# Kernel optimization log

Hardware: AMD Instinct MI355X
Metric: run time of the kernel (lower is better)

Reference implementation:

```python
import jax, jax.numpy as jnp
import numpy as np


def setup_inputs() -> dict:
    key = jax.random.key(0)
    k1, k2, k3, k4 = jax.random.split(key, 4)
    B, S, D = 2, 2048, 1024
    return {
        "X": jax.random.normal(k1, (B, S, D), dtype=jnp.float32),
        "W_q": jax.random.normal(k2, (D, D), dtype=jnp.float32),
        "W_k": jax.random.normal(k3, (D, D), dtype=jnp.float32),
        "W_v": jax.random.normal(k4, (D, D), dtype=jnp.float32),
        "n_heads": 16,
    }


def reference(X, W_q, W_k, W_v, n_heads):
    B, S, D = X.shape
    H = n_heads
    dh = D // H
    # QKV projections, split heads: [B,S,D] -> [H,B,S,dh]
    def split_heads(Y):
        return Y.reshape(B, S, H, dh).transpose(2, 0, 1, 3)
    Q = split_heads(X @ W_q)
    K = split_heads(X @ W_k)
    V = split_heads(X @ W_v)
    scale = 1.0 / jnp.sqrt(jnp.asarray(dh, dtype=X.dtype))
    # [H,B,S,S] attention scores (naive, matches the original)
    scores = jax.nn.softmax(jnp.einsum("hbqd,hbkd->hbqk", Q, K) * scale, axis=-1)
    out = jnp.einsum("hbqk,hbkd->hbqd", scores, V)  # [H,B,S,dh]
    # torch.concat(out, 0) over leading H dim -> [H*B, S, dh]
    return out.reshape(H * B, S, dh)
```

## Files before the change

### kernel.cpp

```cpp
#include <hip/hip_runtime.h>

typedef unsigned short u16;
typedef unsigned int u32;
typedef __bf16 bf16x8 __attribute__((ext_vector_type(8)));
typedef float f32x4 __attribute__((ext_vector_type(4)));
typedef float f32x16 __attribute__((ext_vector_type(16)));

extern "C" __device__ float __ocml_native_exp2_f32(float);

#define WT_HI_E  ((size_t)0)
#define WT_LO_E  ((size_t)3 << 20)
#define X_HI_E   ((size_t)6 << 20)
#define X_LO_E   ((size_t)10 << 20)
#define Q_HI_E   ((size_t)14 << 20)
#define Q_LO_E   ((size_t)18 << 20)
#define K_HI_E   ((size_t)22 << 20)
#define K_LO_E   ((size_t)26 << 20)
#define V_HI_E   ((size_t)30 << 20)

__device__ __forceinline__ u16 bf16_rne(float x) {
  u32 u = __float_as_uint(x);
  u32 r = (u + 0x7fffu + ((u >> 16) & 1u)) >> 16;
  return (u16)r;
}
__device__ __forceinline__ float bf16_f(u16 h) {
  return __uint_as_float(((u32)h) << 16);
}
__device__ __forceinline__ u16 f2bf(float x) {
  __bf16 b = (__bf16)x;
  return __builtin_bit_cast(u16, b);
}

__device__ __forceinline__ void gload16(const u16* g, u16* l) {
  __builtin_amdgcn_global_load_lds(
      (const __attribute__((address_space(1))) void*)g,
      (__attribute__((address_space(3))) void*)l, 16, 0, 0);
}

__global__ __launch_bounds__(256) void k_split(const float* __restrict__ X,
                                               const float* __restrict__ w0,
                                               const float* __restrict__ w1,
                                               const float* __restrict__ w2,
                                               u16* __restrict__ ws) {
  int bid = blockIdx.x;
  if (bid < 2048) {
    u16* xh = ws + X_HI_E;
    u16* xl = ws + X_LO_E;
    size_t i = ((size_t)bid * 256 + threadIdx.x) * 8;
    float4 a = *(const float4*)(X + i);
    float4 b = *(const float4*)(X + i + 4);
    float v[8] = {a.x, a.y, a.z, a.w, b.x, b.y, b.z, b.w};
    u32 Hh[4], Ll[4];
#pragma unroll
    for (int j = 0; j < 4; j++) {
      u16 h0 = f2bf(v[2 * j]);
      u16 h1 = f2bf(v[2 * j + 1]);
      u16 l0 = f2bf(v[2 * j] - bf16_f(h0));
      u16 l1 = f2bf(v[2 * j + 1] - bf16_f(h1));
      Hh[j] = (u32)h0 | ((u32)h1 << 16);
      Ll[j] = (u32)l0 | ((u32)l1 << 16);
    }
    *(uint4*)(xh + i) = make_uint4(Hh[0], Hh[1], Hh[2], Hh[3]);
    *(uint4*)(xl + i) = make_uint4(Ll[0], Ll[1], Ll[2], Ll[3]);
  } else {
    int wb = bid - 2048;
    int z = wb >> 8;
    int rem = wb & 255;
    int by = (rem >> 4) * 64, bx = (rem & 15) * 64;
    const float* W = (z == 0) ? w0 : ((z == 1) ? w1 : w2);
    u16* th = ws + WT_HI_E + (size_t)z * (1u << 20);
    u16* tl = ws + WT_LO_E + (size_t)z * (1u << 20);
    __shared__ float tile[64][65];
    int tx = threadIdx.x & 15, ty = threadIdx.x >> 4;
#pragma unroll
    for (int i = 0; i < 4; i++) {
      int r = ty + i * 16;
      float4 v = *(const float4*)(W + (size_t)(by + r) * 1024 + bx + tx * 4);
      tile[r][tx * 4 + 0] = v.x;
      tile[r][tx * 4 + 1] = v.y;
      tile[r][tx * 4 + 2] = v.z;
      tile[r][tx * 4 + 3] = v.w;
    }
    __syncthreads();
#pragma unroll
    for (int p = 0; p < 2; p++) {
      int t = threadIdx.x + 256 * p;
      int kc = t & 7, nl = t >> 3;
      u32 Hh[4], Ll[4];
#pragma unroll
      for (int u = 0; u < 4; u++) {
        float v0 = tile[kc * 8 + 2 * u][nl];
        float v1 = tile[kc * 8 + 2 * u + 1][nl];
        u16 h0 = f2bf(v0);
        u16 h1 = f2bf(v1);
        u16 l0 = f2bf(v0 - bf16_f(h0));
        u16 l1 = f2bf(v1 - bf16_f(h1));
        Hh[u] = (u32)h0 | ((u32)h1 << 16);
        Ll[u] = (u32)l0 | ((u32)l1 << 16);
      }
      size_t o = (size_t)(bx + nl) * 1024 + by + kc * 8;
      *(uint4*)(th + o) = make_uint4(Hh[0], Hh[1], Hh[2], Hh[3]);
      *(uint4*)(tl + o) = make_uint4(Ll[0], Ll[1], Ll[2], Ll[3]);
    }
  }
}

__global__ __launch_bounds__(256, 4) void k_proj(u16* __restrict__ ws) {
  int id = blockIdx.x;
  int xcd = id & 7;
  int loc = id >> 3;
  int m_loc = loc & 7;
  int rest = loc >> 3;
  int n_blk = rest & 7, z = rest >> 3;
  int M0 = (xcd * 8 + m_loc) * 64;
  int N0 = n_blk * 128;

  const u16* Xh = ws + X_HI_E;
  const u16* Xl = ws + X_LO_E;
  const u16* Wh = ws + WT_HI_E + (size_t)z * (1u << 20);
  const u16* Wl = ws + WT_LO_E + (size_t)z * (1u << 20);
  u16* dsth = ws + ((z == 0) ? Q_HI_E : ((z == 1) ? K_HI_E : V_HI_E));
  u16* dstl = (z == 0) ? (ws + Q_LO_E) : ((z == 1) ? (ws + K_LO_E) : (u16*)0);

  __shared__ u16 smem[12288];
  u16* sXh = smem;
  u16* sXl = smem + 2048;
  u16* sWh = smem + 4096;
  u16* sWl = smem + 8192;

  int tid = threadIdx.x, lane = tid & 63, w = tid >> 6;
  int quad = lane >> 4, l16 = lane & 15;
  int mb = (w & 1) * 32, nb = (w >> 1) * 64;

  const f32x4 z4 = {0.f, 0.f, 0.f, 0.f};
  f32x4 acc[4][2];
#pragma unroll
  for (int j = 0; j < 4; j++)
#pragma unroll
    for (int i = 0; i < 2; i++) acc[j][i] = z4;

  int xrow = tid >> 2, xq8 = tid & 3;

  for (int kk = 0; kk < 1024; kk += 32) {
    __syncthreads();
    {
      size_t gx = (size_t)(M0 + xrow) * 1024 + kk + xq8 * 8;
      gload16(Xh + gx, &sXh[(size_t)(w * 16) * 32]);
      if (z != 2) gload16(Xl + gx, &sXl[(size_t)(w * 16) * 32]);
#pragma unroll
      for (int j = 0; j < 2; j++) {
        int c = tid + 256 * j;
        int row = c >> 2, q8 = c & 3;
        size_t gw = (size_t)(N0 + row) * 1024 + kk + q8 * 8;
        gload16(Wh + gw, &sWh[(size_t)(j * 64 + w * 16) * 32]);
        if (z != 2) gload16(Wl + gw, &sWl[(size_t)(j * 64 + w * 16) * 32]);
      }
    }
    __syncthreads();
    bf16x8 ah[2], bh[4];
#pragma unroll
    for (int i = 0; i < 2; i++)
      ah[i] = *(const bf16x8*)&sXh[(mb + i * 16 + l16) * 32 + quad * 8];
#pragma unroll
    for (int j = 0; j < 4; j++)
      bh[j] = *(const bf16x8*)&sWh[(nb + j * 16 + l16) * 32 + quad * 8];
    if (z != 2) {
      bf16x8 al[2], bl[4];
#pragma unroll
      for (int i = 0; i < 2; i++)
        al[i] = *(const bf16x8*)&sXl[(mb + i * 16 + l16) * 32 + quad * 8];
#pragma unroll
      for (int j = 0; j < 4; j++)
        bl[j] = *(const bf16x8*)&sWl[(nb + j * 16 + l16) * 32 + quad * 8];
#pragma unroll
      for (int j = 0; j < 4; j++)
#pragma unroll
        for (int i = 0; i < 2; i++) {
          f32x4 c0 = acc[j][i];
          c0 = __builtin_amdgcn_mfma_f32_16x16x32_bf16(bh[j], ah[i], c0, 0, 0, 0);
          c0 = __builtin_amdgcn_mfma_f32_16x16x32_bf16(bh[j], al[i], c0, 0, 0, 0);
          c0 = __builtin_amdgcn_mfma_f32_16x16x32_bf16(bl[j], ah[i], c0, 0, 0, 0);
          acc[j][i] = c0;
        }
    } else {
#pragma unroll
      for (int j = 0; j < 4; j++)
#pragma unroll
        for (int i = 0; i < 2; i++)
          acc[j][i] = __builtin_amdgcn_mfma_f32_16x16x32_bf16(ah[i], bh[j], acc[j][i], 0, 0, 0);
    }
  }

  __syncthreads();
  int b = M0 >> 11, S0 = M0 & 2047;

  if (z != 2) {
    u16* my = smem + (size_t)w * 2048;
    int hh = (N0 + nb) >> 6;
    int sbase = S0 + mb;
    float qscale = (z == 0) ? (0.125f * 1.4426950408889634f) : 1.0f;
#pragma unroll
    for (int pass = 0; pass < 2; pass++) {
      u16* dst = pass ? dstl : dsth;
#pragma unroll
      for (int j = 0; j < 4; j++)
#pragma unroll
        for (int i = 0; i < 2; i++) {
          int dl = j * 16 + quad * 4;
          int sl = i * 16 + l16;
          u16 e[4];
#pragma unroll
          for (int r = 0; r < 4; r++) {
            float y = acc[j][i][r] * qscale;
            u16 hv = bf16_rne(y);
            e[r] = pass ? bf16_rne(y - bf16_f(hv)) : hv;
          }
          int elem = sl * 64 + (((dl >> 3) ^ (sl & 7)) << 3) + (dl & 7);
          *(uint2*)&my[elem] = make_uint2((u32)e[0] | ((u32)e[1] << 16),
                                          (u32)e[2] | ((u32)e[3] << 16));
        }
#pragma unroll
      for (int t = 0; t < 4; t++) {
        int sr = (lane >> 3) + t * 8;
        int p = lane & 7;
        int rc = (z == 1) ? p : (p ^ (sr & 7));
        uint4 v = *(const uint4*)&my[sr * 64 + rc * 8];
        size_t o = ((size_t)(hh * 2 + b) * 2048 + sbase + sr) * 64 + p * 8;
        *(uint4*)&dst[o] = v;
      }
    }
  } else {
#pragma unroll
    for (int j = 0; j < 4; j++)
#pragma unroll
      for (int i = 0; i < 2; i++) {
        int dl = j * 16 + l16;
        int s64 = mb + i * 16 + quad * 4;
        u16 e[4];
#pragma unroll
        for (int r = 0; r < 4; r++) e[r] = bf16_rne(acc[j][i][r]);
        int cp = ((s64 >> 3) & 7) ^ (dl & 7);
        int elem = (w >> 1) * 4096 + dl * 64 + (cp << 3) + (s64 & 7);
        *(uint2*)&smem[elem] = make_uint2((u32)e[0] | ((u32)e[1] << 16),
                                          (u32)e[2] | ((u32)e[3] << 16));
      }
    __syncthreads();
    int half = w >> 1;
    int hh = (N0 + half * 64) >> 6;
#pragma unroll
    for (int t = 0; t < 4; t++) {
      int dr = (w & 1) * 32 + (lane >> 3) + t * 8;
      int p = lane & 7;
      uint4 v = *(const uint4*)&smem[half * 4096 + dr * 64 + p * 8];
      size_t o = ((size_t)(hh * 2 + b) * 64 + dr) * 2048 + S0 + p * 8;
      *(uint4*)&dsth[o] = v;
    }
  }
}

__global__ __launch_bounds__(256, 2) void k_attn(u16* __restrict__ ws,
                                                 float* __restrict__ out) {
  const u16* Qh = ws + Q_HI_E;
  const u16* Ql = ws + Q_LO_E;
  const u16* Kh = ws + K_HI_E;
  const u16* Kl = ws + K_LO_E;
  const u16* Vt = ws + V_HI_E;

  __shared__ u16 sKh[2][64][64], sKl[2][64][64], sVt[2][64][64];

  int id = blockIdx.x;
  int hb = id & 31, qb = id >> 5;
  int tid = threadIdx.x, w = tid >> 6, lane = tid & 63;
  int l31 = lane & 31, h = lane >> 5;
  size_t base = (size_t)hb * (2048 * 64);
  int qw0 = qb * 128 + w * 32;

  int srow = lane >> 3, sch = lane & 7;

  auto stage = [&](int buf, int kt) {
#pragma unroll
    for (int b2 = 0; b2 < 2; b2++) {
      int rr = w * 16 + b2 * 8;
      size_t kg = base + (size_t)(kt + rr + srow) * 64 + sch * 8;
      gload16(Kh + kg, &sKh[buf][rr][0]);
      gload16(Kl + kg, &sKl[buf][rr][0]);
      size_t vg = base + (size_t)(rr + srow) * 2048 + kt + sch * 8;
      gload16(Vt + vg, &sVt[buf][rr][0]);
    }
  };

  stage(0, 0);

  bf16x8 qh[4], ql[4];
#pragma unroll
  for (int ks = 0; ks < 4; ks++) {
    size_t off = base + (size_t)(qw0 + l31) * 64 + ks * 16 + h * 8;
    qh[ks] = *(const bf16x8*)(Qh + off);
    ql[ks] = *(const bf16x8*)(Ql + off);
  }

  f32x16 o[2];
#pragma unroll
  for (int i = 0; i < 16; i++) { o[0][i] = 0.f; o[1][i] = 0.f; }
  float mr = -1e30f, lr = 0.f;

  auto rdA = [&](const u16 t[64][64], int mt, int ks) -> bf16x8 {
    int ch = ((ks * 2 + h) ^ (l31 & 7)) * 8;
    return *(const bf16x8*)&t[mt * 32 + l31][ch];
  };

  for (int it = 0; it < 32; it++) {
    __syncthreads();
    if (it + 1 < 32) stage((it + 1) & 1, (it + 1) * 64);
    int buf = it & 1;

    f32x16 sc[2];
#pragma unroll
    for (int i = 0; i < 16; i++) { sc[0][i] = 0.f; sc[1][i] = 0.f; }
#pragma unroll
    for (int ks = 0; ks < 4; ks++)
#pragma unroll
      for (int mt = 0; mt < 2; mt++) {
        bf16x8 kh = rdA(sKh[buf], mt, ks);
        bf16x8 kl = rdA(sKl[buf], mt, ks);
        sc[mt] = __builtin_amdgcn_mfma_f32_32x32x16_bf16(kh, qh[ks], sc[mt], 0, 0, 0);
        sc[mt] = __builtin_amdgcn_mfma_f32_32x32x16_bf16(kh, ql[ks], sc[mt], 0, 0, 0);
        sc[mt] = __builtin_amdgcn_mfma_f32_32x32x16_bf16(kl, qh[ks], sc[mt], 0, 0, 0);
      }

    float mx = sc[0][0];
#pragma unroll
    for (int i = 0; i < 16; i++) {
      mx = fmaxf(mx, sc[0][i]);
      mx = fmaxf(mx, sc[1][i]);
    }
    mx = fmaxf(mx, __shfl_xor(mx, 32));
    float mnew = fmaxf(mr, mx);
    float alpha = __ocml_native_exp2_f32(mr - mnew);
    mr = mnew;
    float rs = 0.f;
    u32 pk[2][8];
#pragma unroll
    for (int t = 0; t < 2; t++)
#pragma unroll
      for (int i = 0; i < 8; i++) {
        float p0 = __ocml_native_exp2_f32(sc[t][2 * i] - mnew);
        float p1 = __ocml_native_exp2_f32(sc[t][2 * i + 1] - mnew);
        rs += p0 + p1;
        u32 a = __float_as_uint(p0) + 0x8000u;
        u32 b = __float_as_uint(p1) + 0x8000u;
        pk[t][i] = __builtin_amdgcn_perm(b, a, 0x07060302u);
      }
    rs += __shfl_xor(rs, 32);
    lr = lr * alpha + rs;
#pragma unroll
    for (int i = 0; i < 16; i++) {
      o[0][i] *= alpha;
      o[1][i] *= alpha;
    }

#pragma unroll
    for (int ks = 0; ks < 4; ks++) {
      int t = ks >> 1, c = ks & 1;
      u32 b0 = pk[t][c * 4 + 0], b1 = pk[t][c * 4 + 1];
      u32 b2 = pk[t][c * 4 + 2], b3 = pk[t][c * 4 + 3];
      u32 rA = (u32)__shfl_xor((int)(h ? b0 : b2), 32);
      u32 rB = (u32)__shfl_xor((int)(h ? b1 : b3), 32);
      uint4 fb = h ? make_uint4(rA, rB, b2, b3) : make_uint4(b0, b1, rA, rB);
      bf16x8 pfrag = *(bf16x8*)&fb;
#pragma unroll
      for (int mt = 0; mt < 2; mt++) {
        bf16x8 vb = rdA(sVt[buf], mt, ks);
        o[mt] = __builtin_amdgcn_mfma_f32_32x32x16_bf16(vb, pfrag, o[mt], 0, 0, 0);
      }
    }
  }

  float inv = 1.f / lr;
  size_t grow = (size_t)hb * 2048 + qw0 + l31;
#pragma unroll
  for (int mt = 0; mt < 2; mt++)
#pragma unroll
    for (int g2 = 0; g2 < 4; g2++) {
      int d0 = mt * 32 + g2 * 8 + 4 * h;
      float4 v = make_float4(o[mt][g2 * 4 + 0] * inv, o[mt][g2 * 4 + 1] * inv,
                             o[mt][g2 * 4 + 2] * inv, o[mt][g2 * 4 + 3] * inv);
      *(float4*)(out + grow * 64 + d0) = v;
    }
}

extern "C" void kernel_launch(void* const* d_in, const int* in_sizes, int n_in,
                              void* d_out, int out_size, void* d_ws, size_t ws_size,
                              hipStream_t stream) {
  const float* X = (const float*)d_in[0];
  const float* Wq = (const float*)d_in[1];
  const float* Wk = (const float*)d_in[2];
  const float* Wv = (const float*)d_in[3];
  u16* ws = (u16*)d_ws;
  float* out = (float*)d_out;

  k_split<<<dim3(2816), dim3(256), 0, stream>>>(X, Wq, Wk, Wv, ws);
  k_proj<<<dim3(1536), dim3(256), 0, stream>>>(ws);
  k_attn<<<dim3(512), dim3(256), 0, stream>>>(ws, out);
}
```

Before: 229.1 us.

## Software-pipeline attention: triple-buffer K/V, overlap next QK^T with softmax, lazy rescale

Moves K/V staging to a three-deep shared-memory ring and computes the next tile's QK^T scores before the current tile's softmax and PV, so matrix-core work can overlap the exponential and reduction work. Online-softmax rescaling is skipped unless some row's max grows by more than 8 (in log2 units), which removes most alpha multiplies. The max reduction becomes a tree, and s_setprio raises wave priority around the MFMA blocks. In exchange it uses more LDS and more registers (two score buffers), which may reduce occupancy under the two-blocks-per-CU launch bound.

```diff
diff --git a/kernel.cpp b/kernel.cpp
--- a/kernel.cpp
+++ b/kernel.cpp
@@ -266,7 +266,7 @@
   const u16* Kl = ws + K_LO_E;
   const u16* Vt = ws + V_HI_E;
 
-  __shared__ u16 sKh[2][64][64], sKl[2][64][64], sVt[2][64][64];
+  __shared__ u16 sKh[3][64][64], sKl[3][64][64], sVt[3][64][64];
 
   int id = blockIdx.x;
   int hb = id & 31, qb = id >> 5;
@@ -290,6 +290,7 @@
   };
 
   stage(0, 0);
+  stage(1, 64);
 
   bf16x8 qh[4], ql[4];
 #pragma unroll
@@ -299,24 +300,15 @@
     ql[ks] = *(const bf16x8*)(Ql + off);
   }
 
-  f32x16 o[2];
-#pragma unroll
-  for (int i = 0; i < 16; i++) { o[0][i] = 0.f; o[1][i] = 0.f; }
-  float mr = -1e30f, lr = 0.f;
-
   auto rdA = [&](const u16 t[64][64], int mt, int ks) -> bf16x8 {
     int ch = ((ks * 2 + h) ^ (l31 & 7)) * 8;
     return *(const bf16x8*)&t[mt * 32 + l31][ch];
   };
 
-  for (int it = 0; it < 32; it++) {
-    __syncthreads();
-    if (it + 1 < 32) stage((it + 1) & 1, (it + 1) * 64);
-    int buf = it & 1;
-
-    f32x16 sc[2];
+  auto qkt = [&](int buf, f32x16* sc) {
 #pragma unroll
     for (int i = 0; i < 16; i++) { sc[0][i] = 0.f; sc[1][i] = 0.f; }
+    __builtin_amdgcn_s_setprio(1);
 #pragma unroll
     for (int ks = 0; ks < 4; ks++)
 #pragma unroll
@@ -327,38 +319,61 @@
         sc[mt] = __builtin_amdgcn_mfma_f32_32x32x16_bf16(kh, ql[ks], sc[mt], 0, 0, 0);
         sc[mt] = __builtin_amdgcn_mfma_f32_32x32x16_bf16(kl, qh[ks], sc[mt], 0, 0, 0);
       }
-
-    float mx = sc[0][0];
-#pragma unroll
-    for (int i = 0; i < 16; i++) {
-      mx = fmaxf(mx, sc[0][i]);
-      mx = fmaxf(mx, sc[1][i]);
-    }
-    mx = fmaxf(mx, __shfl_xor(mx, 32));
-    float mnew = fmaxf(mr, mx);
-    float alpha = __ocml_native_exp2_f32(mr - mnew);
-    mr = mnew;
+    __builtin_amdgcn_s_setprio(0);
+  };
+
+  f32x16 o[2];
+#pragma unroll
+  for (int i = 0; i < 16; i++) { o[0][i] = 0.f; o[1][i] = 0.f; }
+  float mr = -1e30f, lr = 0.f;
+
+  f32x16 scA[2], scB[2];
+
+  __syncthreads();
+  qkt(0, scA);
+
+  auto body = [&](int it, f32x16* scc, f32x16* scn) {
+    __syncthreads();
+    if (it + 2 < 32) stage((it + 2) % 3, (it + 2) * 64);
+    if (it + 1 < 32) qkt((it + 1) % 3, scn);
+
+    float m8[8];
+#pragma unroll
+    for (int i = 0; i < 8; i++)
+      m8[i] = fmaxf(fmaxf(scc[0][2 * i], scc[0][2 * i + 1]),
+                    fmaxf(scc[1][2 * i], scc[1][2 * i + 1]));
+#pragma unroll
+    for (int s = 4; s > 0; s >>= 1)
+#pragma unroll
+      for (int i = 0; i < 4; i++)
+        if (i < s) m8[i] = fmaxf(m8[i], m8[i + s]);
+    float mx = fmaxf(m8[0], __shfl_xor(m8[0], 32));
+    if (!__all(mx - mr <= 8.0f)) {
+      float mnew = fmaxf(mr, mx);
+      float alpha = __ocml_native_exp2_f32(mr - mnew);
+      mr = mnew;
+      lr *= alpha;
+#pragma unroll
+      for (int i = 0; i < 16; i++) { o[0][i] *= alpha; o[1][i] *= alpha; }
+    }
     float rs = 0.f;
     u32 pk[2][8];
 #pragma unroll
     for (int t = 0; t < 2; t++)
 #pragma unroll
       for (int i = 0; i < 8; i++) {
-        float p0 = __ocml_native_exp2_f32(sc[t][2 * i] - mnew);
-        float p1 = __ocml_native_exp2_f32(sc[t][2 * i + 1] - mnew);
+        float p0 = __ocml_native_exp2_f32(scc[t][2 * i] - mr);
+        float p1 = __ocml_native_exp2_f32(scc[t][2 * i + 1] - mr);
         rs += p0 + p1;
         u32 a = __float_as_uint(p0) + 0x8000u;
         u32 b = __float_as_uint(p1) + 0x8000u;
         pk[t][i] = __builtin_amdgcn_perm(b, a, 0x07060302u);
       }
     rs += __shfl_xor(rs, 32);
-    lr = lr * alpha + rs;
-#pragma unroll
-    for (int i = 0; i < 16; i++) {
-      o[0][i] *= alpha;
-      o[1][i] *= alpha;
-    }
-
+    lr += rs;
+
+    int buf = it % 3;
+    __builtin_amdgcn_s_setprio(1);
 #pragma unroll
     for (int ks = 0; ks < 4; ks++) {
       int t = ks >> 1, c = ks & 1;
@@ -374,6 +389,12 @@
         o[mt] = __builtin_amdgcn_mfma_f32_32x32x16_bf16(vb, pfrag, o[mt], 0, 0, 0);
       }
     }
+    __builtin_amdgcn_s_setprio(0);
+  };
+
+  for (int it = 0; it < 32; it += 2) {
+    body(it, scA, scB);
+    body(it + 1, scB, scA);
   }
 
   float inv = 1.f / lr;
```

New measurement: 229.8 us. About the same (+0.3%).

## Split attention KV range in two halves with merge kernel, load K-lo directly

Applied to the files above, without the earlier changes.

The attention kernel now splits the key sequence into two halves (flash-decoding style), doubling the grid to 1024 blocks and writing unnormalized partial outputs plus per-row max/sum, which a new merge kernel combines. The K low-part tile is no longer staged in LDS but read straight from global memory into registers, cutting LDS use so occupancy can rise to 4 blocks per CU. This adds an extra kernel launch and extra global traffic for the partials, and it reuses the workspace region holding the X/W bf16 splits as scratch.

```diff
diff --git a/kernel.cpp b/kernel.cpp
--- a/kernel.cpp
+++ b/kernel.cpp
@@ -17,6 +17,7 @@
 #define K_HI_E   ((size_t)22 << 20)
 #define K_LO_E   ((size_t)26 << 20)
 #define V_HI_E   ((size_t)30 << 20)
+#define ML_BYTE  (17u << 20)
 
 __device__ __forceinline__ u16 bf16_rne(float x) {
   u32 u = __float_as_uint(x);
@@ -258,7 +259,7 @@
   }
 }
 
-__global__ __launch_bounds__(256, 2) void k_attn(u16* __restrict__ ws,
+__global__ __launch_bounds__(256, 4) void k_attn(u16* __restrict__ ws,
                                                  float* __restrict__ out) {
   const u16* Qh = ws + Q_HI_E;
   const u16* Ql = ws + Q_LO_E;
@@ -266,10 +267,11 @@
   const u16* Kl = ws + K_LO_E;
   const u16* Vt = ws + V_HI_E;
 
-  __shared__ u16 sKh[2][64][64], sKl[2][64][64], sVt[2][64][64];
+  __shared__ u16 sKh[2][64][64], sVt[2][64][64];
 
   int id = blockIdx.x;
-  int hb = id & 31, qb = id >> 5;
+  int hb = id & 31, qb = (id >> 5) & 15, half = id >> 9;
+  int kbase = half << 10;
   int tid = threadIdx.x, w = tid >> 6, lane = tid & 63;
   int l31 = lane & 31, h = lane >> 5;
   size_t base = (size_t)hb * (2048 * 64);
@@ -277,13 +279,13 @@
 
   int srow = lane >> 3, sch = lane & 7;
 
-  auto stage = [&](int buf, int kt) {
+  auto stage = [&](int buf, int t) {
+    int kt = kbase + t * 64;
 #pragma unroll
     for (int b2 = 0; b2 < 2; b2++) {
       int rr = w * 16 + b2 * 8;
       size_t kg = base + (size_t)(kt + rr + srow) * 64 + sch * 8;
       gload16(Kh + kg, &sKh[buf][rr][0]);
-      gload16(Kl + kg, &sKl[buf][rr][0]);
       size_t vg = base + (size_t)(rr + srow) * 2048 + kt + sch * 8;
       gload16(Vt + vg, &sVt[buf][rr][0]);
     }
@@ -309,9 +311,19 @@
     return *(const bf16x8*)&t[mt * 32 + l31][ch];
   };
 
-  for (int it = 0; it < 32; it++) {
+  for (int it = 0; it < 16; it++) {
     __syncthreads();
-    if (it + 1 < 32) stage((it + 1) & 1, (it + 1) * 64);
+    int kt = kbase + it * 64;
+    bf16x8 klf[8];
+#pragma unroll
+    for (int ks = 0; ks < 4; ks++)
+#pragma unroll
+      for (int mt = 0; mt < 2; mt++) {
+        int row = kt + mt * 32 + l31;
+        int c2 = ((ks * 2 + h) ^ (row & 7)) * 8;
+        klf[ks * 2 + mt] = *(const bf16x8*)(Kl + base + (size_t)row * 64 + c2);
+      }
+    if (it + 1 < 16) stage((it + 1) & 1, it + 1);
     int buf = it & 1;
 
     f32x16 sc[2];
@@ -322,11 +334,14 @@
 #pragma unroll
       for (int mt = 0; mt < 2; mt++) {
         bf16x8 kh = rdA(sKh[buf], mt, ks);
-        bf16x8 kl = rdA(sKl[buf], mt, ks);
         sc[mt] = __builtin_amdgcn_mfma_f32_32x32x16_bf16(kh, qh[ks], sc[mt], 0, 0, 0);
         sc[mt] = __builtin_amdgcn_mfma_f32_32x32x16_bf16(kh, ql[ks], sc[mt], 0, 0, 0);
-        sc[mt] = __builtin_amdgcn_mfma_f32_32x32x16_bf16(kl, qh[ks], sc[mt], 0, 0, 0);
-      }
+      }
+#pragma unroll
+    for (int ks = 0; ks < 4; ks++)
+#pragma unroll
+      for (int mt = 0; mt < 2; mt++)
+        sc[mt] = __builtin_amdgcn_mfma_f32_32x32x16_bf16(klf[ks * 2 + mt], qh[ks], sc[mt], 0, 0, 0);
 
     float mx = sc[0][0];
 #pragma unroll
@@ -376,17 +391,41 @@
     }
   }
 
-  float inv = 1.f / lr;
+  float* dst = (half == 0) ? out : (float*)ws;
   size_t grow = (size_t)hb * 2048 + qw0 + l31;
 #pragma unroll
   for (int mt = 0; mt < 2; mt++)
 #pragma unroll
     for (int g2 = 0; g2 < 4; g2++) {
       int d0 = mt * 32 + g2 * 8 + 4 * h;
-      float4 v = make_float4(o[mt][g2 * 4 + 0] * inv, o[mt][g2 * 4 + 1] * inv,
-                             o[mt][g2 * 4 + 2] * inv, o[mt][g2 * 4 + 3] * inv);
-      *(float4*)(out + grow * 64 + d0) = v;
-    }
+      float4 v = make_float4(o[mt][g2 * 4 + 0], o[mt][g2 * 4 + 1],
+                             o[mt][g2 * 4 + 2], o[mt][g2 * 4 + 3]);
+      *(float4*)(dst + grow * 64 + d0) = v;
+    }
+  if (h == 0) {
+    float2* ml = (float2*)((char*)ws + ML_BYTE);
+    ml[(size_t)half * 65536 + grow] = make_float2(mr, lr);
+  }
+}
+
+__global__ __launch_bounds__(256) void k_merge(u16* __restrict__ ws,
+                                               float* __restrict__ out) {
+  size_t g = (size_t)blockIdx.x * 256 + threadIdx.x;
+  size_t row = g >> 4;
+  const float2* ml = (const float2*)((const char*)ws + ML_BYTE);
+  float2 a = ml[row];
+  float2 b = ml[65536 + row];
+  float M = fmaxf(a.x, b.x);
+  float e0 = __ocml_native_exp2_f32(a.x - M);
+  float e1 = __ocml_native_exp2_f32(b.x - M);
+  float winv = 1.f / (a.y * e0 + b.y * e1);
+  float4 p0 = ((const float4*)out)[g];
+  float4 p1 = ((const float4*)(const void*)ws)[g];
+  float4 r = make_float4((p0.x * e0 + p1.x * e1) * winv,
+                         (p0.y * e0 + p1.y * e1) * winv,
+                         (p0.z * e0 + p1.z * e1) * winv,
+                         (p0.w * e0 + p1.w * e1) * winv);
+  ((float4*)out)[g] = r;
 }
 
 extern "C" void kernel_launch(void* const* d_in, const int* in_sizes, int n_in,
@@ -401,5 +440,6 @@
 
   k_split<<<dim3(2816), dim3(256), 0, stream>>>(X, Wq, Wk, Wv, ws);
   k_proj<<<dim3(1536), dim3(256), 0, stream>>>(ws);
-  k_attn<<<dim3(512), dim3(256), 0, stream>>>(ws, out);
-}
+  k_attn<<<dim3(1024), dim3(256), 0, stream>>>(ws, out);
+  k_merge<<<dim3(4096), dim3(256), 0, stream>>>(ws, out);
+}
```

Result: slower. 264.8 us (+15.6%).

## Fuse X bf16 hi/lo split into projection kernel with swizzled LDS staging

Applied to the files above, without the earlier changes.

The separate pass that split X into bf16 hi/lo arrays in workspace is removed. The projection kernel now loads fp32 X tiles directly into LDS with an XOR swizzle and converts them to hi/lo bf16 in registers before the MFMAs. W tiles also get an XOR-swizzled LDS layout to cut bank conflicts. This avoids writing and rereading about 16 MB of intermediate X data, at the cost of redoing the conversion in every N-block and z block that reads the same X rows.

```diff
diff --git a/kernel.cpp b/kernel.cpp
--- a/kernel.cpp
+++ b/kernel.cpp
@@ -10,8 +10,6 @@
 
 #define WT_HI_E  ((size_t)0)
 #define WT_LO_E  ((size_t)3 << 20)
-#define X_HI_E   ((size_t)6 << 20)
-#define X_LO_E   ((size_t)10 << 20)
 #define Q_HI_E   ((size_t)14 << 20)
 #define Q_LO_E   ((size_t)18 << 20)
 #define K_HI_E   ((size_t)22 << 20)
@@ -37,75 +35,53 @@
       (__attribute__((address_space(3))) void*)l, 16, 0, 0);
 }
 
-__global__ __launch_bounds__(256) void k_split(const float* __restrict__ X,
-                                               const float* __restrict__ w0,
+__global__ __launch_bounds__(256) void k_split(const float* __restrict__ w0,
                                                const float* __restrict__ w1,
                                                const float* __restrict__ w2,
                                                u16* __restrict__ ws) {
-  int bid = blockIdx.x;
-  if (bid < 2048) {
-    u16* xh = ws + X_HI_E;
-    u16* xl = ws + X_LO_E;
-    size_t i = ((size_t)bid * 256 + threadIdx.x) * 8;
-    float4 a = *(const float4*)(X + i);
-    float4 b = *(const float4*)(X + i + 4);
-    float v[8] = {a.x, a.y, a.z, a.w, b.x, b.y, b.z, b.w};
+  int wb = blockIdx.x;
+  int z = wb >> 8;
+  int rem = wb & 255;
+  int by = (rem >> 4) * 64, bx = (rem & 15) * 64;
+  const float* W = (z == 0) ? w0 : ((z == 1) ? w1 : w2);
+  u16* th = ws + WT_HI_E + (size_t)z * (1u << 20);
+  u16* tl = ws + WT_LO_E + (size_t)z * (1u << 20);
+  __shared__ float tile[64][65];
+  int tx = threadIdx.x & 15, ty = threadIdx.x >> 4;
+#pragma unroll
+  for (int i = 0; i < 4; i++) {
+    int r = ty + i * 16;
+    float4 v = *(const float4*)(W + (size_t)(by + r) * 1024 + bx + tx * 4);
+    tile[r][tx * 4 + 0] = v.x;
+    tile[r][tx * 4 + 1] = v.y;
+    tile[r][tx * 4 + 2] = v.z;
+    tile[r][tx * 4 + 3] = v.w;
+  }
+  __syncthreads();
+#pragma unroll
+  for (int p = 0; p < 2; p++) {
+    int t = threadIdx.x + 256 * p;
+    int kc = t & 7, nl = t >> 3;
     u32 Hh[4], Ll[4];
 #pragma unroll
-    for (int j = 0; j < 4; j++) {
-      u16 h0 = f2bf(v[2 * j]);
-      u16 h1 = f2bf(v[2 * j + 1]);
-      u16 l0 = f2bf(v[2 * j] - bf16_f(h0));
-      u16 l1 = f2bf(v[2 * j + 1] - bf16_f(h1));
-      Hh[j] = (u32)h0 | ((u32)h1 << 16);
-      Ll[j] = (u32)l0 | ((u32)l1 << 16);
-    }
-    *(uint4*)(xh + i) = make_uint4(Hh[0], Hh[1], Hh[2], Hh[3]);
-    *(uint4*)(xl + i) = make_uint4(Ll[0], Ll[1], Ll[2], Ll[3]);
-  } else {
-    int wb = bid - 2048;
-    int z = wb >> 8;
-    int rem = wb & 255;
-    int by = (rem >> 4) * 64, bx = (rem & 15) * 64;
-    const float* W = (z == 0) ? w0 : ((z == 1) ? w1 : w2);
-    u16* th = ws + WT_HI_E + (size_t)z * (1u << 20);
-    u16* tl = ws + WT_LO_E + (size_t)z * (1u << 20);
-    __shared__ float tile[64][65];
-    int tx = threadIdx.x & 15, ty = threadIdx.x >> 4;
-#pragma unroll
-    for (int i = 0; i < 4; i++) {
-      int r = ty + i * 16;
-      float4 v = *(const float4*)(W + (size_t)(by + r) * 1024 + bx + tx * 4);
-      tile[r][tx * 4 + 0] = v.x;
-      tile[r][tx * 4 + 1] = v.y;
-      tile[r][tx * 4 + 2] = v.z;
-      tile[r][tx * 4 + 3] = v.w;
-    }
-    __syncthreads();
-#pragma unroll
-    for (int p = 0; p < 2; p++) {
-      int t = threadIdx.x + 256 * p;
-      int kc = t & 7, nl = t >> 3;
-      u32 Hh[4], Ll[4];
-#pragma unroll
-      for (int u = 0; u < 4; u++) {
-        float v0 = tile[kc * 8 + 2 * u][nl];
-        float v1 = tile[kc * 8 + 2 * u + 1][nl];
-        u16 h0 = f2bf(v0);
-        u16 h1 = f2bf(v1);
-        u16 l0 = f2bf(v0 - bf16_f(h0));
-        u16 l1 = f2bf(v1 - bf16_f(h1));
-        Hh[u] = (u32)h0 | ((u32)h1 << 16);
-        Ll[u] = (u32)l0 | ((u32)l1 << 16);
-      }
-      size_t o = (size_t)(bx + nl) * 1024 + by + kc * 8;
-      *(uint4*)(th + o) = make_uint4(Hh[0], Hh[1], Hh[2], Hh[3]);
-      *(uint4*)(tl + o) = make_uint4(Ll[0], Ll[1], Ll[2], Ll[3]);
-    }
-  }
-}
-
-__global__ __launch_bounds__(256, 4) void k_proj(u16* __restrict__ ws) {
+    for (int u = 0; u < 4; u++) {
+      float v0 = tile[kc * 8 + 2 * u][nl];
+      float v1 = tile[kc * 8 + 2 * u + 1][nl];
+      u16 h0 = f2bf(v0);
+      u16 h1 = f2bf(v1);
+      u16 l0 = f2bf(v0 - bf16_f(h0));
+      u16 l1 = f2bf(v1 - bf16_f(h1));
+      Hh[u] = (u32)h0 | ((u32)h1 << 16);
+      Ll[u] = (u32)l0 | ((u32)l1 << 16);
+    }
+    size_t o = (size_t)(bx + nl) * 1024 + by + kc * 8;
+    *(uint4*)(th + o) = make_uint4(Hh[0], Hh[1], Hh[2], Hh[3]);
+    *(uint4*)(tl + o) = make_uint4(Ll[0], Ll[1], Ll[2], Ll[3]);
+  }
+}
+
+__global__ __launch_bounds__(256, 4) void k_proj(const float* __restrict__ X,
+                                                 u16* __restrict__ ws) {
   int id = blockIdx.x;
   int xcd = id & 7;
   int loc = id >> 3;
@@ -115,16 +91,13 @@
   int M0 = (xcd * 8 + m_loc) * 64;
   int N0 = n_blk * 128;
 
-  const u16* Xh = ws + X_HI_E;
-  const u16* Xl = ws + X_LO_E;
   const u16* Wh = ws + WT_HI_E + (size_t)z * (1u << 20);
   const u16* Wl = ws + WT_LO_E + (size_t)z * (1u << 20);
   u16* dsth = ws + ((z == 0) ? Q_HI_E : ((z == 1) ? K_HI_E : V_HI_E));
   u16* dstl = (z == 0) ? (ws + Q_LO_E) : ((z == 1) ? (ws + K_LO_E) : (u16*)0);
 
   __shared__ u16 smem[12288];
-  u16* sXh = smem;
-  u16* sXl = smem + 2048;
+  float* sXf = (float*)smem;
   u16* sWh = smem + 4096;
   u16* sWl = smem + 8192;
 
@@ -139,39 +112,64 @@
 #pragma unroll
     for (int i = 0; i < 2; i++) acc[j][i] = z4;
 
-  int xrow = tid >> 2, xq8 = tid & 3;
-
   for (int kk = 0; kk < 1024; kk += 32) {
     __syncthreads();
     {
-      size_t gx = (size_t)(M0 + xrow) * 1024 + kk + xq8 * 8;
-      gload16(Xh + gx, &sXh[(size_t)(w * 16) * 32]);
-      if (z != 2) gload16(Xl + gx, &sXl[(size_t)(w * 16) * 32]);
 #pragma unroll
       for (int j = 0; j < 2; j++) {
         int c = tid + 256 * j;
-        int row = c >> 2, q8 = c & 3;
-        size_t gw = (size_t)(N0 + row) * 1024 + kk + q8 * 8;
-        gload16(Wh + gw, &sWh[(size_t)(j * 64 + w * 16) * 32]);
-        if (z != 2) gload16(Wl + gw, &sWl[(size_t)(j * 64 + w * 16) * 32]);
+        int row = c >> 3, q = c & 7;
+        int gq = q ^ (row & 7);
+        const float* src = X + (size_t)(M0 + row) * 1024 + kk + gq * 4;
+        gload16((const u16*)src, &smem[(size_t)(w * 64 + 256 * j) * 8]);
+      }
+#pragma unroll
+      for (int j = 0; j < 2; j++) {
+        int c = tid + 256 * j;
+        int row = c >> 2, q = c & 3;
+        int gq = q ^ ((row >> 1) & 3);
+        size_t gw = (size_t)(N0 + row) * 1024 + kk + gq * 8;
+        gload16(Wh + gw, &sWh[(size_t)(w * 64 + 256 * j) * 8]);
+        if (z != 2) gload16(Wl + gw, &sWl[(size_t)(w * 64 + 256 * j) * 8]);
       }
     }
     __syncthreads();
-    bf16x8 ah[2], bh[4];
-#pragma unroll
-    for (int i = 0; i < 2; i++)
-      ah[i] = *(const bf16x8*)&sXh[(mb + i * 16 + l16) * 32 + quad * 8];
-#pragma unroll
-    for (int j = 0; j < 4; j++)
-      bh[j] = *(const bf16x8*)&sWh[(nb + j * 16 + l16) * 32 + quad * 8];
+
+    bf16x8 bh[4];
+#pragma unroll
+    for (int j = 0; j < 4; j++) {
+      int row = nb + j * 16 + l16;
+      bh[j] = *(const bf16x8*)&sWh[row * 32 + (quad ^ ((row >> 1) & 3)) * 8];
+    }
+    bf16x8 ah[2], al[2];
+#pragma unroll
+    for (int i = 0; i < 2; i++) {
+      int row = mb + i * 16 + l16;
+      const float* rp = sXf + row * 32;
+      int r7 = row & 7;
+      f32x4 xa = *(const f32x4*)(rp + ((quad * 2) ^ r7) * 4);
+      f32x4 xb = *(const f32x4*)(rp + ((quad * 2 + 1) ^ r7) * 4);
+      bf16x8 hv, lv;
+#pragma unroll
+      for (int e = 0; e < 4; e++) {
+        __bf16 h0 = (__bf16)xa[e];
+        hv[e] = h0;
+        lv[e] = (__bf16)(xa[e] - (float)h0);
+        __bf16 h1 = (__bf16)xb[e];
+        hv[4 + e] = h1;
+        lv[4 + e] = (__bf16)(xb[e] - (float)h1);
+      }
+      ah[i] = hv;
+      al[i] = lv;
+    }
+
     if (z != 2) {
-      bf16x8 al[2], bl[4];
-#pragma unroll
-      for (int i = 0; i < 2; i++)
-        al[i] = *(const bf16x8*)&sXl[(mb + i * 16 + l16) * 32 + quad * 8];
-#pragma unroll
-      for (int j = 0; j < 4; j++)
-        bl[j] = *(const bf16x8*)&sWl[(nb + j * 16 + l16) * 32 + quad * 8];
+      bf16x8 bl[4];
+#pragma unroll
+      for (int j = 0; j < 4; j++) {
+        int row = nb + j * 16 + l16;
+        bl[j] = *(const bf16x8*)&sWl[row * 32 + (quad ^ ((row >> 1) & 3)) * 8];
+      }
 #pragma unroll
       for (int j = 0; j < 4; j++)
 #pragma unroll
@@ -277,14 +275,14 @@
 
   int srow = lane >> 3, sch = lane & 7;
 
-  auto stage = [&](int buf, int kt) {
+  auto stage = [&](int buf, int t) {
 #pragma unroll
     for (int b2 = 0; b2 < 2; b2++) {
       int rr = w * 16 + b2 * 8;
-      size_t kg = base + (size_t)(kt + rr + srow) * 64 + sch * 8;
+      size_t kg = base + (size_t)(t * 64 + rr + srow) * 64 + sch * 8;
       gload16(Kh + kg, &sKh[buf][rr][0]);
       gload16(Kl + kg, &sKl[buf][rr][0]);
-      size_t vg = base + (size_t)(rr + srow) * 2048 + kt + sch * 8;
+      size_t vg = base + (size_t)(rr + srow) * 2048 + t * 64 + sch * 8;
       gload16(Vt + vg, &sVt[buf][rr][0]);
     }
   };
@@ -311,7 +309,7 @@
 
   for (int it = 0; it < 32; it++) {
     __syncthreads();
-    if (it + 1 < 32) stage((it + 1) & 1, (it + 1) * 64);
+    if (it + 1 < 32) stage((it + 1) & 1, it + 1);
     int buf = it & 1;
 
     f32x16 sc[2];
@@ -399,7 +397,7 @@
   u16* ws = (u16*)d_ws;
   float* out = (float*)d_out;
 
-  k_split<<<dim3(2816), dim3(256), 0, stream>>>(X, Wq, Wk, Wv, ws);
-  k_proj<<<dim3(1536), dim3(256), 0, stream>>>(ws);
+  k_split<<<dim3(768), dim3(256), 0, stream>>>(Wq, Wk, Wv, ws);
+  k_proj<<<dim3(1536), dim3(256), 0, stream>>>(X, ws);
   k_attn<<<dim3(512), dim3(256), 0, stream>>>(ws, out);
 }
```

Result: no change. 226.3 us (-1.2%).
